# Optimization experiments

Hardware: AMD Instinct MI355X
Metric: run time of the kernel (lower is better)

Reference implementation:

```python
import jax, jax.numpy as jnp
import numpy as np

N_NODES = 100000
N_EDGES = 1600000
N_GRAPHS = 64
F_IN = 256
HID = 256
PROJ = 128
L = 4


def setup_inputs() -> dict:
    key = jax.random.key(0)
    ks = jax.random.split(key, 12)
    x = jax.random.normal(ks[0], (N_NODES, F_IN), dtype=jnp.float32)
    edge_index = jax.random.randint(ks[1], (2, N_EDGES), 0, N_NODES)
    batch = jnp.sort(jax.random.randint(ks[2], (N_NODES,), 0, N_GRAPHS))
    s = 0.05
    # SAGEConv per layer: lin_l (applied to mean-aggregated neighbors, with bias)
    # and lin_r (applied to root node, no bias). All layers are 256->256, stacked.
    Wl = jax.random.normal(ks[3], (L, HID, HID), dtype=jnp.float32) * s
    bl = jax.random.normal(ks[4], (L, HID), dtype=jnp.float32) * s
    Wr = jax.random.normal(ks[5], (L, HID, HID), dtype=jnp.float32) * s
    gamma = jnp.ones((L, HID), dtype=jnp.float32)
    beta = jnp.zeros((L, HID), dtype=jnp.float32)
    W1 = jax.random.normal(ks[6], (HID, HID), dtype=jnp.float32) * s
    b1 = jnp.zeros((HID,), dtype=jnp.float32)
    W2 = jax.random.normal(ks[7], (HID, PROJ), dtype=jnp.float32) * s
    b2 = jnp.zeros((PROJ,), dtype=jnp.float32)
    return {"x": x, "edge_index": edge_index, "batch": batch,
            "Wl": Wl, "bl": bl, "Wr": Wr, "gamma": gamma, "beta": beta,
            "W1": W1, "b1": b1, "W2": W2, "b2": b2}


def _segment_mean(vals, seg_ids, num_segments):
    sums = jax.ops.segment_sum(vals, seg_ids, num_segments=num_segments)
    cnt = jax.ops.segment_sum(jnp.ones((vals.shape[0],), vals.dtype), seg_ids,
                              num_segments=num_segments)
    return sums / jnp.maximum(cnt, 1.0)[:, None]


def reference(x, edge_index, batch, Wl, bl, Wr, gamma, beta, W1, b1, W2, b2):
    src, dst = edge_index[0], edge_index[1]
    eps = 1e-5
    h = x
    for i in range(L):
        # SAGEConv: mean-aggregate neighbor features, then lin_l(aggr) + lin_r(root)
        aggr = _segment_mean(h[src], dst, N_NODES)          # [N, HID]
        h = aggr @ Wl[i] + bl[i] + h @ Wr[i]
        # BatchNorm1d (training-mode batch statistics, biased variance)
        mu = jnp.mean(h, axis=0)
        var = jnp.mean(jnp.square(h - mu), axis=0)
        h = (h - mu) * jax.lax.rsqrt(var + eps) * gamma[i] + beta[i]
        h = jax.nn.relu(h)
        # dropout omitted (inference / deterministic reference)
    g = _segment_mean(h, batch, N_GRAPHS)                   # [G, HID]
    z = jax.nn.relu(g @ W1 + b1) @ W2 + b2                  # [G, PROJ]
    # F.normalize(z, dim=1): L2 normalize with eps clamp
    norm = jnp.maximum(jnp.linalg.norm(z, axis=1, keepdims=True), 1e-12)
    return z / norm
```

## Files before the change

kernel.cpp:

```cpp
#include <hip/hip_runtime.h>

#define N_NODES 100000
#define M_PAD   100096
#define N_MBLK  782
#define N_EDGES 1600000
#define N_GRAPHS 64
#define HID 256
#define PROJ 128
#define NLAYERS 4

#define EBUF_STRIDE 8192
#define N_BUCKETS ((N_NODES + 255) / 256)
#define CSR_BLK 1024
#define EPT 10
#define CSR_NBLK ((N_EDGES + CSR_BLK * EPT - 1) / (CSR_BLK * EPT))
#define SENT 0xFFFFFFFFu

typedef unsigned short u16;
typedef unsigned long long u64;
typedef __attribute__((ext_vector_type(8))) short bf16x8;
typedef __attribute__((ext_vector_type(4))) float f32x4;
typedef __attribute__((ext_vector_type(2))) float vf2;

__device__ __forceinline__ float b2f(u16 u) {
  return __uint_as_float(((unsigned)u) << 16);
}
__device__ __forceinline__ float b2f_lo(unsigned u) {
  return __uint_as_float(u << 16);
}
__device__ __forceinline__ float b2f_hi(unsigned u) {
  return __uint_as_float(u & 0xFFFF0000u);
}
__device__ __forceinline__ u16 f2b(float f) {
  unsigned u = __float_as_uint(f);
  u = (u + 0x7FFF + ((u >> 16) & 1)) >> 16;
  return (u16)u;
}
__device__ __forceinline__ void gload16(const void* g, void* l) {
  __builtin_amdgcn_global_load_lds((const __attribute__((address_space(1))) void*)g,
                                   (__attribute__((address_space(3))) void*)l, 16, 0, 0);
}
__device__ __forceinline__ unsigned pack_fp8x4(float a, float b, float c, float d) {
  int v = __builtin_amdgcn_cvt_pk_fp8_f32(a, b, 0, false);
  v = __builtin_amdgcn_cvt_pk_fp8_f32(c, d, v, true);
  return (unsigned)v;
}
__device__ __forceinline__ void accf8(float* a, unsigned w) {
  vf2 lo = __builtin_amdgcn_cvt_pk_f32_fp8((int)w, false);
  vf2 hi = __builtin_amdgcn_cvt_pk_f32_fp8((int)w, true);
  a[0] += lo.x; a[1] += lo.y; a[2] += hi.x; a[3] += hi.y;
}

__global__ __launch_bounds__(1024) void bucket_scatter(
    const int* __restrict__ src, const int* __restrict__ dst,
    u64* __restrict__ bfill64, uint2* __restrict__ ebuf) {
  __shared__ int lhist[N_BUCKETS];
  __shared__ int lbase[N_BUCKETS];
  int t = threadIdx.x;
  int e0 = blockIdx.x * (CSR_BLK * EPT) + t;
  for (int i = t; i < N_BUCKETS; i += CSR_BLK) lhist[i] = 0;
  __syncthreads();
  int sv[EPT], dv[EPT];
#pragma unroll
  for (int j = 0; j < EPT; j++) {
    int e = e0 + j * CSR_BLK;
    if (e < N_EDGES) {
      sv[j] = src[e];
      dv[j] = dst[e];
      atomicAdd(&lhist[dv[j] >> 8], 1);
    } else {
      dv[j] = -1;
      sv[j] = 0;
    }
  }
  __syncthreads();
  for (int i = t; i < N_BUCKETS; i += CSR_BLK) {
    int c = lhist[i];
    if (c > 0) {
      int rounded = (c + 7) & ~7;
      u64 old = atomicAdd(&bfill64[(size_t)i * 8],
                          ((u64)rounded << 32) | (u64)c);
      int base = (int)(old >> 32);
      lbase[i] = base;
      for (int k = c; k < rounded; k++) {
        int p = base + k;
        if (p < EBUF_STRIDE) {
          uint2 q; q.x = 0; q.y = SENT;
          ebuf[(size_t)i * EBUF_STRIDE + p] = q;
        }
      }
      lhist[i] = 0;
    }
  }
  __syncthreads();
#pragma unroll
  for (int j = 0; j < EPT; j++) {
    if (dv[j] >= 0) {
      int b = dv[j] >> 8;
      int p = lbase[b] + atomicAdd(&lhist[b], 1);
      if (p < EBUF_STRIDE) {
        uint2 q;
        q.x = (unsigned)sv[j];
        q.y = (unsigned)dv[j];
        ebuf[(size_t)b * EBUF_STRIDE + p] = q;
      }
    }
  }
}

__global__ __launch_bounds__(512) void bucket_prefix(
    const u64* __restrict__ bfill64, int* __restrict__ bucket_base,
    int* __restrict__ row_ptr) {
  __shared__ int tile[512];
  int t = threadIdx.x;
  int v = 0;
  if (t < N_BUCKETS) {
    u64 w = bfill64[(size_t)t * 8];
    v = (int)(w & 0xFFFFFFFFull);
    if ((int)(w >> 32) > EBUF_STRIDE) v = min(v, EBUF_STRIDE);
  }
  tile[t] = v;
  __syncthreads();
  for (int off = 1; off < 512; off <<= 1) {
    int add = (t >= off) ? tile[t - off] : 0;
    __syncthreads();
    tile[t] += add;
    __syncthreads();
  }
  if (t < N_BUCKETS) bucket_base[t] = tile[t] - v;
  if (t == N_BUCKETS - 1) row_ptr[N_NODES] = tile[t];
}

__global__ __launch_bounds__(1024) void csr_build(
    const uint2* __restrict__ ebuf, const u64* __restrict__ bfill64,
    const int* __restrict__ bucket_base, int* __restrict__ row_ptr,
    float* __restrict__ inv_cnt, int* __restrict__ col) {
  __shared__ int hist[256];
  __shared__ int nscan[256];
  __shared__ int cursor[256];
  int b = blockIdx.x;
  int t = threadIdx.x;
  int nalloc = min((int)(bfill64[(size_t)b * 8] >> 32), EBUF_STRIDE);
  int bbase = bucket_base[b];
  if (t < 256) hist[t] = 0;
  __syncthreads();
  uint2 q[8];
#pragma unroll
  for (int k = 0; k < 8; k++) {
    int i = t + k * CSR_BLK;
    q[k].x = 0; q[k].y = SENT;
    if (i < nalloc) {
      q[k] = ebuf[(size_t)b * EBUF_STRIDE + i];
      if (q[k].y != SENT) atomicAdd(&hist[q[k].y & 255], 1);
    }
  }
  __syncthreads();
  if (t < 256) nscan[t] = hist[t];
  __syncthreads();
  for (int off = 1; off < 256; off <<= 1) {
    int add = 0;
    if (t < 256 && t >= off) add = nscan[t - off];
    __syncthreads();
    if (t < 256) nscan[t] += add;
    __syncthreads();
  }
  int nb = min(256, N_NODES - b * 256);
  if (t < 256) {
    int excl = nscan[t] - hist[t];
    cursor[t] = excl;
    if (t < nb) {
      row_ptr[b * 256 + t] = bbase + excl;
      inv_cnt[b * 256 + t] = 1.0f / fmaxf((float)hist[t], 1.0f);
    }
  }
  __syncthreads();
#pragma unroll
  for (int k = 0; k < 8; k++) {
    if (q[k].y != SENT) {
      int l = (int)(q[k].y & 255);
      int pos = bbase + atomicAdd(&cursor[l], 1);
      col[pos] = (int)q[k].x;
    }
  }
}

__global__ __launch_bounds__(256) void convert_x(const float4* __restrict__ x,
                                                 ushort4* __restrict__ hb,
                                                 unsigned* __restrict__ h8) {
  int i = blockIdx.x * blockDim.x + threadIdx.x;
  float4 v = x[i];
  ushort4 o;
  o.x = f2b(v.x); o.y = f2b(v.y); o.z = f2b(v.z); o.w = f2b(v.w);
  hb[i] = o;
  h8[i] = pack_fp8x4(v.x, v.y, v.z, v.w);
}

__global__ __launch_bounds__(256) void convert_w(const float* __restrict__ Wl,
                                                 const float* __restrict__ Wr,
                                                 u16* __restrict__ Wt) {
  int idx = blockIdx.x * blockDim.x + threadIdx.x;
  int l = idx >> 17;
  int r = idx & ((1 << 17) - 1);
  int n = r >> 9;
  int k = r & 511;
  float v = (k < 256) ? Wl[(size_t)l * 65536 + k * 256 + n]
                      : Wr[(size_t)l * 65536 + (k - 256) * 256 + n];
  Wt[idx] = f2b(v);
}

__global__ __launch_bounds__(256) void aggregate_fp8(
    const unsigned char* __restrict__ h8, const int* __restrict__ row_ptr,
    const int* __restrict__ col, const float* __restrict__ inv_cnt,
    u16* __restrict__ aggr) {
  int node = blockIdx.x * 4 + (threadIdx.x >> 6);
  int lane = threadIdx.x & 63;
  int half = lane >> 5, l32 = lane & 31;
  int r0 = row_ptr[node], r1 = row_ptr[node + 1];
  float a[8] = {0.f, 0.f, 0.f, 0.f, 0.f, 0.f, 0.f, 0.f};
  int e = r0 + half;
  for (; e + 14 < r1; e += 16) {
    int s[8];
#pragma unroll
    for (int j = 0; j < 8; j++) s[j] = col[e + 2 * j];
    uint2 v[8];
#pragma unroll
    for (int j = 0; j < 8; j++)
      v[j] = *((const uint2*)(h8 + (size_t)s[j] * HID) + l32);
#pragma unroll
    for (int j = 0; j < 8; j++) { accf8(a, v[j].x); accf8(a + 4, v[j].y); }
  }
  for (; e + 6 < r1; e += 8) {
    int s0 = col[e], s1 = col[e + 2], s2 = col[e + 4], s3 = col[e + 6];
    uint2 v0 = *((const uint2*)(h8 + (size_t)s0 * HID) + l32);
    uint2 v1 = *((const uint2*)(h8 + (size_t)s1 * HID) + l32);
    uint2 v2 = *((const uint2*)(h8 + (size_t)s2 * HID) + l32);
    uint2 v3 = *((const uint2*)(h8 + (size_t)s3 * HID) + l32);
    accf8(a, v0.x); accf8(a + 4, v0.y);
    accf8(a, v1.x); accf8(a + 4, v1.y);
    accf8(a, v2.x); accf8(a + 4, v2.y);
    accf8(a, v3.x); accf8(a + 4, v3.y);
  }
  for (; e < r1; e += 2) {
    int s0 = col[e];
    uint2 v0 = *((const uint2*)(h8 + (size_t)s0 * HID) + l32);
    accf8(a, v0.x); accf8(a + 4, v0.y);
  }
#pragma unroll
  for (int j = 0; j < 8; j++) a[j] += __shfl_xor(a[j], 32, 64);
  if (half == 0) {
    float inv = inv_cnt[node];
    uint4 o;
    o.x = (unsigned)f2b(a[0] * inv) | ((unsigned)f2b(a[1] * inv) << 16);
    o.y = (unsigned)f2b(a[2] * inv) | ((unsigned)f2b(a[3] * inv) << 16);
    o.z = (unsigned)f2b(a[4] * inv) | ((unsigned)f2b(a[5] * inv) << 16);
    o.w = (unsigned)f2b(a[6] * inv) | ((unsigned)f2b(a[7] * inv) << 16);
    *((uint4*)(aggr + (size_t)node * HID) + l32) = o;
  }
}

__global__ __launch_bounds__(256, 2) void gemm_fused(
    const u16* hb, const u16* __restrict__ aggr,
    const u16* __restrict__ Bt, u16* hpre,
    float* __restrict__ psum) {
  __shared__ u16 smem[128 * 32 + 256 * 32];
  __shared__ float bns[4][8][16][2];
  u16* As = smem;
  u16* Bs = smem + 128 * 32;
  u16* ep = smem;

  int tid = threadIdx.x;
  int wid = tid >> 6, lane = tid & 63;
  int m0 = blockIdx.x * 128;
  int q = lane >> 4, c = lane & 15;
  int wm = (wid >> 1) * 64, wn = (wid & 1) * 128;

  f32x4 zero = {0.f, 0.f, 0.f, 0.f};
  f32x4 acc[4][8];
#pragma unroll
  for (int mi = 0; mi < 4; mi++)
#pragma unroll
    for (int ni = 0; ni < 8; ni++) acc[mi][ni] = zero;

  int srowA0 = wid * 32 + (lane >> 2);
  int cgA0 = (lane & 3) ^ ((srowA0 >> 1) & 3);
  int srowA1 = srowA0 + 16;
  int cgA1 = (lane & 3) ^ ((srowA1 >> 1) & 3);
  int srowB[4], cgB[4];
#pragma unroll
  for (int j = 0; j < 4; j++) {
    srowB[j] = j * 64 + wid * 16 + (lane >> 2);
    cgB[j] = (lane & 3) ^ ((srowB[j] >> 1) & 3);
  }

  int aoff[4], boff[8];
#pragma unroll
  for (int mi = 0; mi < 4; mi++) {
    int row = wm + mi * 16 + c;
    aoff[mi] = row * 32 + ((q ^ ((row >> 1) & 3)) << 3);
  }
#pragma unroll
  for (int ni = 0; ni < 8; ni++) {
    int row = wn + ni * 16 + c;
    boff[ni] = row * 32 + ((q ^ ((row >> 1) & 3)) << 3);
  }

  for (int k0 = 0; k0 < 512; k0 += 32) {
    const u16* Asrc = (k0 < 256) ? aggr : hb;
    int ksrc = k0 & 255;
    gload16(Asrc + ((size_t)(m0 + srowA0) * HID + ksrc + cgA0 * 8), &As[(wid * 32) * 32]);
    gload16(Asrc + ((size_t)(m0 + srowA1) * HID + ksrc + cgA1 * 8), &As[(wid * 32 + 16) * 32]);
#pragma unroll
    for (int j = 0; j < 4; j++)
      gload16(Bt + ((size_t)srowB[j] * 512 + k0 + cgB[j] * 8), &Bs[(j * 64 + wid * 16) * 32]);
    __syncthreads();
    bf16x8 af[4], bfr[8];
#pragma unroll
    for (int mi = 0; mi < 4; mi++) af[mi] = *(const bf16x8*)&As[aoff[mi]];
#pragma unroll
    for (int ni = 0; ni < 8; ni++) bfr[ni] = *(const bf16x8*)&Bs[boff[ni]];
#pragma unroll
    for (int mi = 0; mi < 4; mi++)
#pragma unroll
      for (int ni = 0; ni < 8; ni++)
        acc[mi][ni] = __builtin_amdgcn_mfma_f32_16x16x32_bf16(af[mi], bfr[ni],
                                                              acc[mi][ni], 0, 0, 0);
    __syncthreads();
  }

  int rh = wid >> 1;
#pragma unroll
  for (int mi = 0; mi < 4; mi++) {
#pragma unroll
    for (int r = 0; r < 4; r++) {
      int r16 = q * 4 + r;
#pragma unroll
      for (int ni = 0; ni < 8; ni++)
        ep[(rh * 16 + r16) * 256 + wn + ni * 16 + c] = f2b(acc[mi][ni][r]);
    }
    __syncthreads();
    int u = tid;
#pragma unroll
    for (int j = 0; j < 4; j++, u += 256) {
      int lr = u >> 5;
      int cu = u & 31;
      int gm = m0 + (lr >> 4) * 64 + mi * 16 + (lr & 15);
      if (gm < N_NODES)
        ((uint4*)(hpre + (size_t)gm * HID))[cu] = ((const uint4*)ep)[u];
    }
    __syncthreads();
  }

#pragma unroll
  for (int ni = 0; ni < 8; ni++) {
    float s = 0.f, s2 = 0.f;
#pragma unroll
    for (int mi = 0; mi < 4; mi++) {
#pragma unroll
      for (int r = 0; r < 4; r++) {
        int gm = m0 + wm + mi * 16 + q * 4 + r;
        float v = (gm < N_NODES) ? acc[mi][ni][r] : 0.f;
        s += v;
        s2 += v * v;
      }
    }
    s += __shfl_xor(s, 16, 64);
    s += __shfl_xor(s, 32, 64);
    s2 += __shfl_xor(s2, 16, 64);
    s2 += __shfl_xor(s2, 32, 64);
    if (q == 0) {
      bns[wid][ni][c][0] = s;
      bns[wid][ni][c][1] = s2;
    }
  }
  __syncthreads();
  {
    int wnh = tid >> 7, ni = (tid >> 4) & 7, cc = tid & 15;
    float s = bns[wnh][ni][cc][0] + bns[wnh + 2][ni][cc][0];
    float s2 = bns[wnh][ni][cc][1] + bns[wnh + 2][ni][cc][1];
    int coln = wnh * 128 + ni * 16 + cc;
    psum[(size_t)blockIdx.x * 512 + coln] = s;
    psum[(size_t)blockIdx.x * 512 + 256 + coln] = s2;
  }
}

#define BN_MID 16
__global__ __launch_bounds__(256) void bn_mid(const float* __restrict__ psum,
                                              float* __restrict__ tmp) {
  int b = blockIdx.x;
  int f = threadIdx.x;
  int mb0 = b * 49;
  int mb1 = min(mb0 + 49, N_MBLK);
  float s = 0.f, s2 = 0.f;
  for (int mb = mb0; mb < mb1; mb++) {
    s += psum[(size_t)mb * 512 + f];
    s2 += psum[(size_t)mb * 512 + 256 + f];
  }
  tmp[(size_t)b * 512 + f] = s;
  tmp[(size_t)b * 512 + 256 + f] = s2;
}

__global__ void bn_fin(const float* __restrict__ tmp,
                       const float* __restrict__ gamma,
                       const float* __restrict__ beta,
                       float* __restrict__ ss) {
  int f = threadIdx.x;
  float sum = 0.f, sq = 0.f;
#pragma unroll
  for (int b = 0; b < BN_MID; b++) {
    sum += tmp[(size_t)b * 512 + f];
    sq += tmp[(size_t)b * 512 + 256 + f];
  }
  const float invN = 1.0f / (float)N_NODES;
  float mu = sum * invN;
  float ex2 = sq * invN;
  float var = fmaxf(ex2 - mu * mu, 0.f);
  float sc = gamma[f] * rsqrtf(var + 1e-5f);
  ss[f] = sc;
  ss[HID + f] = beta[f] - mu * sc;
}

__global__ __launch_bounds__(256) void bn_apply_fused(const uint4* hpre,
                                                      const float* __restrict__ ss,
                                                      uint4* hout,
                                                      uint2* __restrict__ h8out) {
  int idx0 = blockIdx.x * blockDim.x + threadIdx.x;
  int cb = (idx0 & 31) * 8;
  float sc[8], sh[8];
#pragma unroll
  for (int j = 0; j < 8; j++) { sc[j] = ss[cb + j]; sh[j] = ss[HID + cb + j]; }
  const int total = N_NODES * 32;
  const int step = gridDim.x * blockDim.x;
  for (int i = idx0; i < total; i += step) {
    uint4 v = hpre[i];
    unsigned vv[4] = {v.x, v.y, v.z, v.w};
    unsigned o[4];
    float f[8];
#pragma unroll
    for (int j = 0; j < 4; j++) {
      float lo = fmaxf(fmaf(b2f_lo(vv[j]), sc[2 * j], sh[2 * j]), 0.f);
      float hi = fmaxf(fmaf(b2f_hi(vv[j]), sc[2 * j + 1], sh[2 * j + 1]), 0.f);
      f[2 * j] = lo;
      f[2 * j + 1] = hi;
      o[j] = (unsigned)f2b(lo) | ((unsigned)f2b(hi) << 16);
    }
    uint4 ov = {o[0], o[1], o[2], o[3]};
    hout[i] = ov;
    uint2 q;
    q.x = pack_fp8x4(f[0], f[1], f[2], f[3]);
    q.y = pack_fp8x4(f[4], f[5], f[6], f[7]);
    h8out[i] = q;
  }
}

__global__ __launch_bounds__(256) void pool_partial(
    const u16* __restrict__ hpre, const float* __restrict__ ss,
    const int* __restrict__ batch, float* __restrict__ partial) {
  __shared__ float red[256][9];
  int g = blockIdx.x;
  int i = blockIdx.y;
  int t = threadIdx.x;
  int a = 0, b = N_NODES;
  while (a < b) { int m = (a + b) >> 1; if (batch[m] < g) a = m + 1; else b = m; }
  int lo = a;
  b = N_NODES;
  while (a < b) { int m = (a + b) >> 1; if (batch[m] < g + 1) a = m + 1; else b = m; }
  int hi = a;
  int len = hi - lo;
  int clen = (len + 7) >> 3;
  int c0 = lo + i * clen;
  int c1 = min(c0 + clen, hi);

  int rs = t >> 5, cu = t & 31;
  int cb = cu * 8;
  float scv[8], shv[8];
#pragma unroll
  for (int j = 0; j < 8; j++) { scv[j] = ss[cb + j]; shv[j] = ss[HID + cb + j]; }
  float acc[8] = {0.f, 0.f, 0.f, 0.f, 0.f, 0.f, 0.f, 0.f};
  for (int r = c0 + rs; r < c1; r += 8) {
    uint4 v = *((const uint4*)(hpre + (size_t)r * HID) + cu);
    unsigned vv[4] = {v.x, v.y, v.z, v.w};
#pragma unroll
    for (int j = 0; j < 4; j++) {
      acc[2 * j]     += fmaxf(fmaf(b2f_lo(vv[j]), scv[2 * j], shv[2 * j]), 0.f);
      acc[2 * j + 1] += fmaxf(fmaf(b2f_hi(vv[j]), scv[2 * j + 1], shv[2 * j + 1]), 0.f);
    }
  }
#pragma unroll
  for (int j = 0; j < 8; j++) red[t][j] = acc[j];
  __syncthreads();
  int cc = t >> 3, j = t & 7;
  float sum = 0.f;
#pragma unroll
  for (int k = 0; k < 8; k++) sum += red[k * 32 + cc][j];
  partial[((size_t)g * 8 + i) * 256 + t] = sum;
}

__global__ __launch_bounds__(256) void pool_mlp_final(
    const float* __restrict__ partial, const int* __restrict__ batch,
    const float* __restrict__ W1, const float* __restrict__ b1,
    const float* __restrict__ W2, const float* __restrict__ b2,
    float* __restrict__ out) {
  __shared__ float gs[HID];
  __shared__ float ts[HID];
  __shared__ float rn[PROJ];
  int g = blockIdx.x;
  int t = threadIdx.x;
  int a = 0, b = N_NODES;
  while (a < b) { int m = (a + b) >> 1; if (batch[m] < g) a = m + 1; else b = m; }
  int lo = a;
  b = N_NODES;
  while (a < b) { int m = (a + b) >> 1; if (batch[m] < g + 1) a = m + 1; else b = m; }
  int len = a - lo;

  float sum = 0.f;
#pragma unroll
  for (int i = 0; i < 8; i++) sum += partial[((size_t)g * 8 + i) * 256 + t];
  float inv = 1.0f / fmaxf((float)len, 1.0f);
  gs[t] = sum * inv;
  __syncthreads();

  float s = b1[t];
  for (int k = 0; k < HID; k++) s = fmaf(gs[k], W1[(size_t)k * HID + t], s);
  ts[t] = fmaxf(s, 0.f);
  __syncthreads();
  float z = 0.f;
  if (t < PROJ) {
    z = b2[t];
    for (int k = 0; k < HID; k++) z = fmaf(ts[k], W2[(size_t)k * PROJ + t], z);
    rn[t] = z * z;
  }
  __syncthreads();
  for (int off = PROJ / 2; off > 0; off >>= 1) {
    if (t < off) rn[t] += rn[t + off];
    __syncthreads();
  }
  float norm = fmaxf(sqrtf(rn[0]), 1e-12f);
  if (t < PROJ) out[(size_t)g * PROJ + t] = z / norm;
}

extern "C" void kernel_launch(void* const* d_in, const int* in_sizes, int n_in,
                              void* d_out, int out_size, void* d_ws, size_t ws_size,
                              hipStream_t stream) {
  const float* x = (const float*)d_in[0];
  const int* ei = (const int*)d_in[1];
  const int* src = ei;
  const int* dst = ei + N_EDGES;
  const int* batch = (const int*)d_in[2];
  const float* Wl = (const float*)d_in[3];
  const float* Wr = (const float*)d_in[5];
  const float* gamma = (const float*)d_in[6];
  const float* beta = (const float*)d_in[7];
  const float* W1 = (const float*)d_in[8];
  const float* b1 = (const float*)d_in[9];
  const float* W2 = (const float*)d_in[10];
  const float* b2 = (const float*)d_in[11];
  float* out = (float*)d_out;

  char* p = (char*)d_ws;
  const size_t HB = (size_t)M_PAD * HID * sizeof(u16);
  u16* h = (u16*)p;      p += HB;
  u16* aggr = (u16*)p;   p += HB;
  unsigned char* h8 = (unsigned char*)p; p += (size_t)M_PAD * HID;
  u16* Wt = (u16*)p;     p += (size_t)NLAYERS * 512 * HID * sizeof(u16);
  int* col = (int*)p;    p += (size_t)N_EDGES * sizeof(int);
  int* row_ptr = (int*)p; p += 400016;
  float* inv_cnt = (float*)p; p += (size_t)N_NODES * sizeof(float);
  float* psum = (float*)p;    p += (size_t)N_MBLK * 512 * sizeof(float);
  float* tmp = (float*)p;     p += (size_t)BN_MID * 512 * sizeof(float);
  float* ss = (float*)p;      p += 512 * sizeof(float);
  float* partial = (float*)p; p += (size_t)N_GRAPHS * 8 * 256 * sizeof(float);
  uint2* ebuf = (uint2*)p;    p += (size_t)N_BUCKETS * EBUF_STRIDE * sizeof(uint2);

  u64* bfill64 = (u64*)aggr;
  int* bucket_base = (int*)(bfill64 + (size_t)N_BUCKETS * 8);

  hipMemsetAsync(bfill64, 0, (size_t)N_BUCKETS * 8 * sizeof(u64), stream);
  bucket_scatter<<<CSR_NBLK, CSR_BLK, 0, stream>>>(src, dst, bfill64, ebuf);
  bucket_prefix<<<1, 512, 0, stream>>>(bfill64, bucket_base, row_ptr);
  csr_build<<<N_BUCKETS, CSR_BLK, 0, stream>>>(ebuf, bfill64, bucket_base,
                                               row_ptr, inv_cnt, col);

  convert_x<<<N_NODES / 4, 256, 0, stream>>>((const float4*)x, (ushort4*)h,
                                             (unsigned*)h8);
  convert_w<<<(NLAYERS * 512 * HID) / 256, 256, 0, stream>>>(Wl, Wr, Wt);

  for (int l = 0; l < NLAYERS; l++) {
    aggregate_fp8<<<N_NODES / 4, 256, 0, stream>>>(h8, row_ptr, col, inv_cnt, aggr);
    gemm_fused<<<N_MBLK, 256, 0, stream>>>(h, aggr, Wt + (size_t)l * 512 * HID,
                                           h, psum);
    bn_mid<<<BN_MID, 256, 0, stream>>>(psum, tmp);
    bn_fin<<<1, 256, 0, stream>>>(tmp, gamma + (size_t)l * HID,
                                  beta + (size_t)l * HID, ss);
    if (l < NLAYERS - 1) {
      bn_apply_fused<<<2048, 256, 0, stream>>>((const uint4*)h, ss, (uint4*)h,
                                               (uint2*)h8);
    }
  }

  pool_partial<<<dim3(N_GRAPHS, 8), 256, 0, stream>>>(h, ss, batch, partial);
  pool_mlp_final<<<N_GRAPHS, 256, 0, stream>>>(partial, batch, W1, b1, W2, b2, out);
}
```

Baseline: 849.3 us.

## Switch SAGE layer GEMM operands to FP8 and drop bf16 activation copies

Activations, aggregated features and weights are now stored in FP8 (e4m3), and the fused GEMM uses fp8 MFMA instructions with a 64-byte K tile instead of bf16. The bf16 copy of h is no longer written by convert or BN-apply, and aggregate writes half as many bytes. This cuts memory traffic in aggregate, GEMM and BN-apply, and gives higher MFMA throughput. The cost is precision: the root-node input and the weights lose bf16 accuracy, which may push the output error toward tolerance.

```diff
diff --git a/kernel.cpp b/kernel.cpp
--- a/kernel.cpp
+++ b/kernel.cpp
@@ -18,13 +18,9 @@
 
 typedef unsigned short u16;
 typedef unsigned long long u64;
-typedef __attribute__((ext_vector_type(8))) short bf16x8;
 typedef __attribute__((ext_vector_type(4))) float f32x4;
 typedef __attribute__((ext_vector_type(2))) float vf2;
 
-__device__ __forceinline__ float b2f(u16 u) {
-  return __uint_as_float(((unsigned)u) << 16);
-}
 __device__ __forceinline__ float b2f_lo(unsigned u) {
   return __uint_as_float(u << 16);
 }
@@ -184,34 +180,35 @@
   }
 }
 
-__global__ __launch_bounds__(256) void convert_x(const float4* __restrict__ x,
-                                                 ushort4* __restrict__ hb,
-                                                 unsigned* __restrict__ h8) {
+__global__ __launch_bounds__(256) void convert_x8(const float4* __restrict__ x,
+                                                  unsigned* __restrict__ h8) {
   int i = blockIdx.x * blockDim.x + threadIdx.x;
   float4 v = x[i];
-  ushort4 o;
-  o.x = f2b(v.x); o.y = f2b(v.y); o.z = f2b(v.z); o.w = f2b(v.w);
-  hb[i] = o;
   h8[i] = pack_fp8x4(v.x, v.y, v.z, v.w);
 }
 
-__global__ __launch_bounds__(256) void convert_w(const float* __restrict__ Wl,
-                                                 const float* __restrict__ Wr,
-                                                 u16* __restrict__ Wt) {
+__global__ __launch_bounds__(256) void convert_w8(const float* __restrict__ Wl,
+                                                  const float* __restrict__ Wr,
+                                                  unsigned* __restrict__ Wt8) {
   int idx = blockIdx.x * blockDim.x + threadIdx.x;
-  int l = idx >> 17;
-  int r = idx & ((1 << 17) - 1);
-  int n = r >> 9;
-  int k = r & 511;
-  float v = (k < 256) ? Wl[(size_t)l * 65536 + k * 256 + n]
-                      : Wr[(size_t)l * 65536 + (k - 256) * 256 + n];
-  Wt[idx] = f2b(v);
+  int l = idx >> 15;
+  int r = idx & 32767;
+  int n = r >> 7;
+  int k4 = (r & 127) * 4;
+  float v[4];
+#pragma unroll
+  for (int j = 0; j < 4; j++) {
+    int k = k4 + j;
+    v[j] = (k < 256) ? Wl[(size_t)l * 65536 + k * 256 + n]
+                     : Wr[(size_t)l * 65536 + (k - 256) * 256 + n];
+  }
+  Wt8[idx] = pack_fp8x4(v[0], v[1], v[2], v[3]);
 }
 
 __global__ __launch_bounds__(256) void aggregate_fp8(
     const unsigned char* __restrict__ h8, const int* __restrict__ row_ptr,
     const int* __restrict__ col, const float* __restrict__ inv_cnt,
-    u16* __restrict__ aggr) {
+    unsigned char* __restrict__ aggr8) {
   int node = blockIdx.x * 4 + (threadIdx.x >> 6);
   int lane = threadIdx.x & 63;
   int half = lane >> 5, l32 = lane & 31;
@@ -249,24 +246,22 @@
   for (int j = 0; j < 8; j++) a[j] += __shfl_xor(a[j], 32, 64);
   if (half == 0) {
     float inv = inv_cnt[node];
-    uint4 o;
-    o.x = (unsigned)f2b(a[0] * inv) | ((unsigned)f2b(a[1] * inv) << 16);
-    o.y = (unsigned)f2b(a[2] * inv) | ((unsigned)f2b(a[3] * inv) << 16);
-    o.z = (unsigned)f2b(a[4] * inv) | ((unsigned)f2b(a[5] * inv) << 16);
-    o.w = (unsigned)f2b(a[6] * inv) | ((unsigned)f2b(a[7] * inv) << 16);
-    *((uint4*)(aggr + (size_t)node * HID) + l32) = o;
-  }
-}
-
-__global__ __launch_bounds__(256, 2) void gemm_fused(
-    const u16* hb, const u16* __restrict__ aggr,
-    const u16* __restrict__ Bt, u16* hpre,
+    uint2 o;
+    o.x = pack_fp8x4(a[0] * inv, a[1] * inv, a[2] * inv, a[3] * inv);
+    o.y = pack_fp8x4(a[4] * inv, a[5] * inv, a[6] * inv, a[7] * inv);
+    *((uint2*)(aggr8 + (size_t)node * HID) + l32) = o;
+  }
+}
+
+__global__ __launch_bounds__(256, 2) void gemm_fused_fp8(
+    const unsigned char* __restrict__ a8, const unsigned char* __restrict__ h8,
+    const unsigned char* __restrict__ Bt8, u16* __restrict__ hpre,
     float* __restrict__ psum) {
-  __shared__ u16 smem[128 * 32 + 256 * 32];
+  __shared__ unsigned char smem[128 * 64 + 256 * 64];
   __shared__ float bns[4][8][16][2];
-  u16* As = smem;
-  u16* Bs = smem + 128 * 32;
-  u16* ep = smem;
+  unsigned char* As = smem;
+  unsigned char* Bs = smem + 128 * 64;
+  u16* ep = (u16*)smem;
 
   int tid = threadIdx.x;
   int wid = tid >> 6, lane = tid & 63;
@@ -292,38 +287,57 @@
     cgB[j] = (lane & 3) ^ ((srowB[j] >> 1) & 3);
   }
 
-  int aoff[4], boff[8];
+  int aoff[4][2], boff[8][2];
 #pragma unroll
   for (int mi = 0; mi < 4; mi++) {
     int row = wm + mi * 16 + c;
-    aoff[mi] = row * 32 + ((q ^ ((row >> 1) & 3)) << 3);
+    int x = (row >> 1) & 3;
+#pragma unroll
+    for (int kk = 0; kk < 2; kk++) {
+      int chunk = kk * 2 + (q >> 1);
+      aoff[mi][kk] = row * 64 + ((chunk ^ x) << 4) + ((q & 1) << 3);
+    }
   }
 #pragma unroll
   for (int ni = 0; ni < 8; ni++) {
     int row = wn + ni * 16 + c;
-    boff[ni] = row * 32 + ((q ^ ((row >> 1) & 3)) << 3);
-  }
-
-  for (int k0 = 0; k0 < 512; k0 += 32) {
-    const u16* Asrc = (k0 < 256) ? aggr : hb;
+    int x = (row >> 1) & 3;
+#pragma unroll
+    for (int kk = 0; kk < 2; kk++) {
+      int chunk = kk * 2 + (q >> 1);
+      boff[ni][kk] = row * 64 + ((chunk ^ x) << 4) + ((q & 1) << 3);
+    }
+  }
+
+  for (int k0 = 0; k0 < 512; k0 += 64) {
+    const unsigned char* Asrc = (k0 < 256) ? a8 : h8;
     int ksrc = k0 & 255;
-    gload16(Asrc + ((size_t)(m0 + srowA0) * HID + ksrc + cgA0 * 8), &As[(wid * 32) * 32]);
-    gload16(Asrc + ((size_t)(m0 + srowA1) * HID + ksrc + cgA1 * 8), &As[(wid * 32 + 16) * 32]);
+    gload16(Asrc + ((size_t)(m0 + srowA0) * HID + ksrc + cgA0 * 16), &As[(wid * 32) * 64]);
+    gload16(Asrc + ((size_t)(m0 + srowA1) * HID + ksrc + cgA1 * 16), &As[(wid * 32 + 16) * 64]);
 #pragma unroll
     for (int j = 0; j < 4; j++)
-      gload16(Bt + ((size_t)srowB[j] * 512 + k0 + cgB[j] * 8), &Bs[(j * 64 + wid * 16) * 32]);
-    __syncthreads();
-    bf16x8 af[4], bfr[8];
-#pragma unroll
-    for (int mi = 0; mi < 4; mi++) af[mi] = *(const bf16x8*)&As[aoff[mi]];
-#pragma unroll
-    for (int ni = 0; ni < 8; ni++) bfr[ni] = *(const bf16x8*)&Bs[boff[ni]];
+      gload16(Bt8 + ((size_t)srowB[j] * 512 + k0 + cgB[j] * 16), &Bs[(j * 64 + wid * 16) * 64]);
+    __syncthreads();
+    long long af[4][2], bfr[8][2];
+#pragma unroll
+    for (int mi = 0; mi < 4; mi++) {
+      af[mi][0] = *(const long long*)&As[aoff[mi][0]];
+      af[mi][1] = *(const long long*)&As[aoff[mi][1]];
+    }
+#pragma unroll
+    for (int ni = 0; ni < 8; ni++) {
+      bfr[ni][0] = *(const long long*)&Bs[boff[ni][0]];
+      bfr[ni][1] = *(const long long*)&Bs[boff[ni][1]];
+    }
 #pragma unroll
     for (int mi = 0; mi < 4; mi++)
 #pragma unroll
-      for (int ni = 0; ni < 8; ni++)
-        acc[mi][ni] = __builtin_amdgcn_mfma_f32_16x16x32_bf16(af[mi], bfr[ni],
-                                                              acc[mi][ni], 0, 0, 0);
+      for (int ni = 0; ni < 8; ni++) {
+        acc[mi][ni] = __builtin_amdgcn_mfma_f32_16x16x32_fp8_fp8(
+            af[mi][0], bfr[ni][0], acc[mi][ni], 0, 0, 0);
+        acc[mi][ni] = __builtin_amdgcn_mfma_f32_16x16x32_fp8_fp8(
+            af[mi][1], bfr[ni][1], acc[mi][ni], 0, 0, 0);
+      }
     __syncthreads();
   }
 
@@ -419,10 +433,9 @@
   ss[HID + f] = beta[f] - mu * sc;
 }
 
-__global__ __launch_bounds__(256) void bn_apply_fused(const uint4* hpre,
-                                                      const float* __restrict__ ss,
-                                                      uint4* hout,
-                                                      uint2* __restrict__ h8out) {
+__global__ __launch_bounds__(256) void bn_apply_h8(const uint4* __restrict__ hpre,
+                                                   const float* __restrict__ ss,
+                                                   uint2* __restrict__ h8out) {
   int idx0 = blockIdx.x * blockDim.x + threadIdx.x;
   int cb = (idx0 & 31) * 8;
   float sc[8], sh[8];
@@ -433,18 +446,12 @@
   for (int i = idx0; i < total; i += step) {
     uint4 v = hpre[i];
     unsigned vv[4] = {v.x, v.y, v.z, v.w};
-    unsigned o[4];
     float f[8];
 #pragma unroll
     for (int j = 0; j < 4; j++) {
-      float lo = fmaxf(fmaf(b2f_lo(vv[j]), sc[2 * j], sh[2 * j]), 0.f);
-      float hi = fmaxf(fmaf(b2f_hi(vv[j]), sc[2 * j + 1], sh[2 * j + 1]), 0.f);
-      f[2 * j] = lo;
-      f[2 * j + 1] = hi;
-      o[j] = (unsigned)f2b(lo) | ((unsigned)f2b(hi) << 16);
-    }
-    uint4 ov = {o[0], o[1], o[2], o[3]};
-    hout[i] = ov;
+      f[2 * j]     = fmaxf(fmaf(b2f_lo(vv[j]), sc[2 * j], sh[2 * j]), 0.f);
+      f[2 * j + 1] = fmaxf(fmaf(b2f_hi(vv[j]), sc[2 * j + 1], sh[2 * j + 1]), 0.f);
+    }
     uint2 q;
     q.x = pack_fp8x4(f[0], f[1], f[2], f[3]);
     q.y = pack_fp8x4(f[4], f[5], f[6], f[7]);
@@ -558,10 +565,11 @@
 
   char* p = (char*)d_ws;
   const size_t HB = (size_t)M_PAD * HID * sizeof(u16);
-  u16* h = (u16*)p;      p += HB;
-  u16* aggr = (u16*)p;   p += HB;
-  unsigned char* h8 = (unsigned char*)p; p += (size_t)M_PAD * HID;
-  u16* Wt = (u16*)p;     p += (size_t)NLAYERS * 512 * HID * sizeof(u16);
+  const size_t H8 = (size_t)M_PAD * HID;
+  u16* hpre = (u16*)p;   p += HB;
+  unsigned char* aggr8 = (unsigned char*)p; p += H8;
+  unsigned char* h8 = (unsigned char*)p;    p += H8;
+  unsigned char* Wt8 = (unsigned char*)p;   p += (size_t)NLAYERS * 512 * HID;
   int* col = (int*)p;    p += (size_t)N_EDGES * sizeof(int);
   int* row_ptr = (int*)p; p += 400016;
   float* inv_cnt = (float*)p; p += (size_t)N_NODES * sizeof(float);
@@ -571,7 +579,7 @@
   float* partial = (float*)p; p += (size_t)N_GRAPHS * 8 * 256 * sizeof(float);
   uint2* ebuf = (uint2*)p;    p += (size_t)N_BUCKETS * EBUF_STRIDE * sizeof(uint2);
 
-  u64* bfill64 = (u64*)aggr;
+  u64* bfill64 = (u64*)hpre;
   int* bucket_base = (int*)(bfill64 + (size_t)N_BUCKETS * 8);
 
   hipMemsetAsync(bfill64, 0, (size_t)N_BUCKETS * 8 * sizeof(u64), stream);
@@ -580,23 +588,23 @@
   csr_build<<<N_BUCKETS, CSR_BLK, 0, stream>>>(ebuf, bfill64, bucket_base,
                                                row_ptr, inv_cnt, col);
 
-  convert_x<<<N_NODES / 4, 256, 0, stream>>>((const float4*)x, (ushort4*)h,
-                                             (unsigned*)h8);
-  convert_w<<<(NLAYERS * 512 * HID) / 256, 256, 0, stream>>>(Wl, Wr, Wt);
+  convert_x8<<<N_NODES / 4, 256, 0, stream>>>((const float4*)x, (unsigned*)h8);
+  convert_w8<<<(NLAYERS * 512 * HID / 4) / 256, 256, 0, stream>>>(Wl, Wr,
+                                                                  (unsigned*)Wt8);
 
   for (int l = 0; l < NLAYERS; l++) {
-    aggregate_fp8<<<N_NODES / 4, 256, 0, stream>>>(h8, row_ptr, col, inv_cnt, aggr);
-    gemm_fused<<<N_MBLK, 256, 0, stream>>>(h, aggr, Wt + (size_t)l * 512 * HID,
-                                           h, psum);
+    aggregate_fp8<<<N_NODES / 4, 256, 0, stream>>>(h8, row_ptr, col, inv_cnt, aggr8);
+    gemm_fused_fp8<<<N_MBLK, 256, 0, stream>>>(aggr8, h8,
+                                               Wt8 + (size_t)l * 512 * HID,
+                                               hpre, psum);
     bn_mid<<<BN_MID, 256, 0, stream>>>(psum, tmp);
     bn_fin<<<1, 256, 0, stream>>>(tmp, gamma + (size_t)l * HID,
                                   beta + (size_t)l * HID, ss);
     if (l < NLAYERS - 1) {
-      bn_apply_fused<<<2048, 256, 0, stream>>>((const uint4*)h, ss, (uint4*)h,
-                                               (uint2*)h8);
-    }
-  }
-
-  pool_partial<<<dim3(N_GRAPHS, 8), 256, 0, stream>>>(h, ss, batch, partial);
+      bn_apply_h8<<<2048, 256, 0, stream>>>((const uint4*)hpre, ss, (uint2*)h8);
+    }
+  }
+
+  pool_partial<<<dim3(N_GRAPHS, 8), 256, 0, stream>>>(hpre, ss, batch, partial);
   pool_mlp_final<<<N_GRAPHS, 256, 0, stream>>>(partial, batch, W1, b1, W2, b2, out);
 }
```

After: 783.6 us. 7.7% less time.
